# Kernel tuning notes

Measured on AMD Instinct MI355X. Metric: run time of the kernel, lower is better.

Reference implementation:

```python
import jax, jax.numpy as jnp
import numpy as np

N_TICKS = 550
N_PMTS = 12
SI = 47  # SiPM grid is 47x47 = 2209
BIN_SIGMA = 0.1
GAUSS_NORM = 1.0 / (BIN_SIGMA * 2.5066282746)


def _dense_init(k, fan_in, fan_out):
    lim = float(np.sqrt(6.0 / (fan_in + fan_out)))  # glorot_uniform (keras Dense default)
    W = jax.random.uniform(k, (fan_in, fan_out), jnp.float32, -lim, lim)
    b = jnp.zeros((fan_out,), jnp.float32)
    return W, b


def setup_inputs() -> dict:
    key = jax.random.key(0)
    ks = jax.random.split(key, 10)
    B, N = 4, 8192  # events x electrons-per-event (ragged list densified)
    xy = jax.random.normal(ks[0], (B, N, 2), jnp.float32)
    z = jax.random.uniform(ks[1], (B, N, 1), jnp.float32, minval=0.0, maxval=549.0)
    electrons = jnp.concatenate([xy, z], axis=-1)  # [B, N, 3] = (x, y, z_ticks)
    weight = jax.random.uniform(ks[2], (B, N), jnp.float32)  # lifetime survival weight
    Wp1, bp1 = _dense_init(ks[3], 2, 28)
    Wp2, bp2 = _dense_init(ks[4], 28, N_PMTS)
    Ws1, bs1 = _dense_init(ks[5], 2, 64)
    Ws2, bs2 = _dense_init(ks[6], 64, 128)
    Ws3, bs3 = _dense_init(ks[7], 128, 256)
    Ws4, bs4 = _dense_init(ks[8], 256, SI * SI)
    pmt_scale = jnp.ones((N_PMTS,), jnp.float32)
    si_scale = jnp.ones((SI * SI,), jnp.float32)
    return dict(electrons=electrons, weight=weight,
                Wp1=Wp1, bp1=bp1, Wp2=Wp2, bp2=bp2, pmt_scale=pmt_scale,
                Ws1=Ws1, bs1=bs1, Ws2=Ws2, bs2=bs2, Ws3=Ws3, bs3=bs3,
                Ws4=Ws4, bs4=bs4, si_scale=si_scale)


def reference(electrons, weight, Wp1, bp1, Wp2, bp2, pmt_scale,
              Ws1, bs1, Ws2, bs2, Ws3, bs3, Ws4, bs4, si_scale):
    B = electrons.shape[0]
    xy = electrons[..., 0:2]            # [B, N, 2]
    z = electrons[..., 2]               # [B, N] in tick units
    # tf.linspace(0.5, n_ticks-0.5, 550) == bin centers
    ticks = jnp.arange(N_TICKS, dtype=electrons.dtype) + 0.5  # [T]
    # per-electron Gaussian over time ticks, scaled by lifetime weight: [B, N, T]
    exp_values = (GAUSS_NORM
                  * jnp.exp(-(ticks - z[..., None]) ** 2 / BIN_SIGMA)
                  * weight[..., None])
    # PMT response MLP: 2 -> 28 -> 12, sigmoid activations
    h = jax.nn.sigmoid(xy @ Wp1 + bp1)
    pmt_resp = jax.nn.sigmoid(h @ Wp2 + bp2) * pmt_scale ** 2    # [B, N, 12]
    # sparse(hist)^T @ response, then transpose -> [B, 12, T]
    pmt_result = jnp.einsum('bnt,bnp->bpt', exp_values, pmt_resp)
    # SiPM response MLP: 2 -> 64 -> 128 -> 256 -> 2209, sigmoid activations
    s = jax.nn.sigmoid(xy @ Ws1 + bs1)
    s = jax.nn.sigmoid(s @ Ws2 + bs2)
    s = jax.nn.sigmoid(s @ Ws3 + bs3)
    sipm_resp = jax.nn.sigmoid(s @ Ws4 + bs4) * si_scale ** 2    # [B, N, 2209]
    sipm_result = jnp.einsum('bnt,bns->bst', exp_values, sipm_resp)  # [B, 2209, T]
    sipm_result = sipm_result.reshape(B, SI, SI, N_TICKS)
    return pmt_result, sipm_result
```

## Files before the change

### kernel.cpp

```cpp
#include <hip/hip_runtime.h>

typedef short short8 __attribute__((ext_vector_type(8)));
typedef short short4v __attribute__((ext_vector_type(4)));
typedef float f32x4 __attribute__((ext_vector_type(4)));

#define NT 550
#define NS 2209
#define NP 12
#define NBK 69
#define SC_NGRP 18
#define SC_GBK 4
#define SC_TW 32
#define NSG 139
#define G1_CPB 8
#define GNRM 3.9894228040143f

typedef unsigned short bfu;

__device__ __forceinline__ bfu f2bf(float f) {
    unsigned int u = __float_as_uint(f);
    unsigned int r = (u + 0x7fffu + ((u >> 16) & 1u)) >> 16;
    return (bfu)r;
}

__device__ __forceinline__ float sigm(float x) {
    return __builtin_amdgcn_rcpf(1.0f + __expf(-x));
}

__global__ void k_prep(const float* __restrict__ W2, const float* __restrict__ W3,
                       const float* __restrict__ W4,
                       bfu* __restrict__ w2h, bfu* __restrict__ w3h, bfu* __restrict__ w4h) {
    int id = blockIdx.x * 256 + threadIdx.x;
    if (id < 8192) {
        int c = id >> 6, k = id & 63;
        w2h[id] = f2bf(W2[k * 128 + c]);
    } else if (id < 8192 + 32768) {
        int j = id - 8192;
        int c = j >> 7, k = j & 127;
        w3h[j] = f2bf(W3[k * 256 + c]);
    } else {
        int j = id - 40960;
        int s = j >> 8, k = j & 255;
        w4h[j] = f2bf(s < NS ? W4[k * NS + s] : 0.0f);
    }
}

__global__ void k_count(const float* __restrict__ el, int* __restrict__ counts) {
    int id = blockIdx.x * 256 + threadIdx.x;
    float z = el[id * 3 + 2];
    int bk = (int)(z * 0.125f);
    bk = bk < 0 ? 0 : (bk > NBK - 1 ? NBK - 1 : bk);
    atomicAdd(&counts[(id >> 13) * NBK + bk], 1);
}

__global__ void k_scan(const int* __restrict__ counts, int* __restrict__ offs) {
    __shared__ int a[512];
    int tid = threadIdx.x;
    int v = (tid < 4 * NBK) ? counts[tid] : 0;
    a[tid] = v;
    __syncthreads();
    for (int s = 1; s < 512; s <<= 1) {
        int t = (tid >= s) ? a[tid - s] : 0;
        __syncthreads();
        a[tid] += t;
        __syncthreads();
    }
    if (tid < 4 * NBK) offs[tid] = a[tid] - v;
}

__global__ void k_scatter(const float* __restrict__ el, const float* __restrict__ wt,
                          const int* __restrict__ offs, int* __restrict__ cur,
                          int* __restrict__ inv, float4* __restrict__ elp) {
    int id = blockIdx.x * 256 + threadIdx.x;
    float x = el[id * 3], y = el[id * 3 + 1], z = el[id * 3 + 2];
    int bk = (int)(z * 0.125f);
    bk = bk < 0 ? 0 : (bk > NBK - 1 ? NBK - 1 : bk);
    int key = (id >> 13) * NBK + bk;
    int pos = offs[key] + atomicAdd(&cur[key], 1);
    inv[id] = pos;
    elp[pos] = make_float4(x, y, z, wt[id]);
}

__global__ __launch_bounds__(256, 1) void k_mlp(
    const float* __restrict__ el,
    const float* __restrict__ Ws1, const float* __restrict__ bs1,
    const float* __restrict__ bs2, const float* __restrict__ bs3,
    const bfu* __restrict__ w2h, const bfu* __restrict__ w3h,
    const int* __restrict__ inv, bfu* __restrict__ s3p) {

    __shared__ __align__(16) bfu bufA[32768];
    __shared__ __align__(16) bfu w3t[32768];
    __shared__ float xyb[256];
    __shared__ float s1w[128];
    __shared__ float b1s[64], b2s[128], b3s[256];

    bfu* h1t = bufA;
    bfu* w2t = bufA + 8192;
    bfu* h2t = bufA + 16384;

    const int tid = threadIdx.x;
    const int wv = tid >> 6, ln = tid & 63;
    const int e0 = blockIdx.x * 128;

    if (tid < 128) s1w[tid] = Ws1[tid];
    if (tid < 64) b1s[tid] = bs1[tid];
    if (tid < 128) b2s[tid] = bs2[tid];
    b3s[tid] = bs3[tid];

    if (tid < 128) {
        int e = e0 + tid;
        xyb[tid * 2] = el[e * 3]; xyb[tid * 2 + 1] = el[e * 3 + 1];
    }
    for (int i = 0; i < 4; ++i) {
        int cid = i * 256 + tid;
        int row = cid >> 3, c5 = cid & 7;
        short8 v = *(const short8*)(const void*)&w2h[row * 64 + c5 * 8];
        *(short8*)(void*)&w2t[row * 64 + ((c5 ^ (row & 7)) * 8)] = v;
    }
    for (int i = 0; i < 16; ++i) {
        int cid = i * 256 + tid;
        int row = cid >> 4, c5 = cid & 15;
        short8 v = *(const short8*)(const void*)&w3h[row * 128 + c5 * 8];
        *(short8*)(void*)&w3t[row * 128 + ((c5 ^ (row & 7)) * 8)] = v;
    }
    __syncthreads();

    {
        int n = tid & 127;
        int j0 = (tid >> 7) * 32;
        float xx = xyb[n * 2], yy = xyb[n * 2 + 1];
        for (int jj = 0; jj < 32; ++jj) {
            int j = j0 + jj;
            float h = sigm(xx * s1w[j] + yy * s1w[64 + j] + b1s[j]);
            h1t[n * 64 + (((j >> 3) ^ (n & 7)) * 8) + (j & 7)] = f2bf(h);
        }
    }
    __syncthreads();

    {
        const int mr = (wv >> 1) * 64;
        const int nc = (wv & 1) * 64;
        f32x4 acc[4][4];
        for (int m = 0; m < 4; ++m) for (int nf = 0; nf < 4; ++nf) acc[m][nf] = (f32x4){0.f, 0.f, 0.f, 0.f};
        for (int kk = 0; kk < 2; ++kk) {
            int kc = kk * 4 + (ln >> 4);
            short8 af[4], bf[4];
            for (int m = 0; m < 4; ++m) {
                int row = mr + 16 * m + (ln & 15);
                af[m] = *(const short8*)(const void*)&h1t[row * 64 + ((kc ^ (row & 7)) * 8)];
            }
            for (int nf = 0; nf < 4; ++nf) {
                int c = nc + 16 * nf + (ln & 15);
                bf[nf] = *(const short8*)(const void*)&w2t[c * 64 + ((kc ^ (c & 7)) * 8)];
            }
            for (int m = 0; m < 4; ++m)
                for (int nf = 0; nf < 4; ++nf)
                    acc[m][nf] = __builtin_amdgcn_mfma_f32_16x16x32_bf16(af[m], bf[nf], acc[m][nf], 0, 0, 0);
        }
        for (int m = 0; m < 4; ++m)
            for (int nf = 0; nf < 4; ++nf) {
                int c = nc + 16 * nf + (ln & 15);
                float bb = b2s[c];
                for (int r = 0; r < 4; ++r) {
                    int n = mr + 16 * m + (ln >> 4) * 4 + r;
                    float hh = sigm(acc[m][nf][r] + bb);
                    h2t[n * 128 + (((c >> 3) ^ (n & 7)) * 8) + (c & 7)] = f2bf(hh);
                }
            }
    }
    __syncthreads();

    f32x4 acc3[4][8];
    const int mr3 = (wv >> 1) * 64;
    const int nc3 = (wv & 1) * 128;
    for (int m = 0; m < 4; ++m) for (int nf = 0; nf < 8; ++nf) acc3[m][nf] = (f32x4){0.f, 0.f, 0.f, 0.f};
    for (int kk = 0; kk < 4; ++kk) {
        int kc = kk * 4 + (ln >> 4);
        short8 af[4];
        for (int m = 0; m < 4; ++m) {
            int row = mr3 + 16 * m + (ln & 15);
            af[m] = *(const short8*)(const void*)&h2t[row * 128 + ((kc ^ (row & 7)) * 8)];
        }
        for (int nf = 0; nf < 8; ++nf) {
            int c = nc3 + 16 * nf + (ln & 15);
            short8 bf = *(const short8*)(const void*)&w3t[c * 128 + ((kc ^ (c & 7)) * 8)];
            for (int m = 0; m < 4; ++m)
                acc3[m][nf] = __builtin_amdgcn_mfma_f32_16x16x32_bf16(af[m], bf, acc3[m][nf], 0, 0, 0);
        }
    }
    __syncthreads();
    for (int m = 0; m < 4; ++m)
        for (int nf = 0; nf < 8; ++nf) {
            int c = nc3 + 16 * nf + (ln & 15);
            float bb = b3s[c];
            for (int r = 0; r < 4; ++r) {
                int n = mr3 + 16 * m + (ln >> 4) * 4 + r;
                float ss = sigm(acc3[m][nf][r] + bb);
                bufA[n * 256 + (((c >> 3) ^ (n & 7)) * 8) + (c & 7)] = f2bf(ss);
            }
        }
    __syncthreads();
    for (int i = 0; i < 16; ++i) {
        int cid = i * 256 + tid;
        int row = cid >> 5, c5 = cid & 31;
        short8 v = *(const short8*)(const void*)&bufA[row * 256 + ((c5 ^ (row & 7)) * 8)];
        int dst = inv[e0 + row];
        *(short8*)(void*)&s3p[(size_t)dst * 256 + c5 * 8] = v;
    }
}

__global__ __launch_bounds__(512, 1) void k_g1(
    const float* __restrict__ bs4, const float* __restrict__ sis,
    const bfu* __restrict__ s3p, const bfu* __restrict__ w4h,
    bfu* __restrict__ resp) {

    __shared__ __align__(16) bfu s3t[128 * 256];
    __shared__ __align__(16) bfu rpt[128 * 128];

    const int tid = threadIdx.x;
    const int wv = tid >> 6, ln = tid & 63;
    const int st = blockIdx.x >> 5;
    const int cg = blockIdx.x & 31;
    const int s0 = st * 128;
    const int wn2 = (wv & 1) * 64;
    const int wsg = (wv >> 1) * 32;

    short8 bfr[2][8];
    float bssr[2], si2r[2];
#pragma unroll
    for (int nf = 0; nf < 2; ++nf) {
        int scol = s0 + wsg + 16 * nf + (ln & 15);
        const bfu* wp = &w4h[(size_t)scol * 256 + (ln >> 4) * 8];
#pragma unroll
        for (int kk = 0; kk < 8; ++kk)
            bfr[nf][kk] = *(const short8*)(const void*)&wp[kk * 32];
        bssr[nf] = (scol < NS) ? bs4[scol] : 0.0f;
        float sc = (scol < NS) ? sis[scol] : 0.0f;
        si2r[nf] = sc * sc;
    }

    const int rowS = tid >> 2;
    const int gq = tid & 3;
    const int r3 = rowS & 7;
    short8 rg0, rg1, rg2, rg3, rg4, rg5, rg6, rg7;

    {
        const bfu* p = s3p + ((size_t)(cg * G1_CPB) * 128 + rowS) * 256 + gq * 8;
        rg0 = *(const short8*)(const void*)&p[0];
        rg1 = *(const short8*)(const void*)&p[32];
        rg2 = *(const short8*)(const void*)&p[64];
        rg3 = *(const short8*)(const void*)&p[96];
        rg4 = *(const short8*)(const void*)&p[128];
        rg5 = *(const short8*)(const void*)&p[160];
        rg6 = *(const short8*)(const void*)&p[192];
        rg7 = *(const short8*)(const void*)&p[224];
    }

    for (int c = 0; c < G1_CPB; ++c) {
        {
            bfu* drow = s3t + rowS * 256;
            *(short8*)(void*)&drow[(((0 * 4 + gq) ^ r3) * 8)] = rg0;
            *(short8*)(void*)&drow[(((1 * 4 + gq) ^ r3) * 8)] = rg1;
            *(short8*)(void*)&drow[(((2 * 4 + gq) ^ r3) * 8)] = rg2;
            *(short8*)(void*)&drow[(((3 * 4 + gq) ^ r3) * 8)] = rg3;
            *(short8*)(void*)&drow[(((4 * 4 + gq) ^ r3) * 8)] = rg4;
            *(short8*)(void*)&drow[(((5 * 4 + gq) ^ r3) * 8)] = rg5;
            *(short8*)(void*)&drow[(((6 * 4 + gq) ^ r3) * 8)] = rg6;
            *(short8*)(void*)&drow[(((7 * 4 + gq) ^ r3) * 8)] = rg7;
        }
        __syncthreads();
        if (c + 1 < G1_CPB) {
            const bfu* p = s3p + ((size_t)(cg * G1_CPB + c + 1) * 128 + rowS) * 256 + gq * 8;
            rg0 = *(const short8*)(const void*)&p[0];
            rg1 = *(const short8*)(const void*)&p[32];
            rg2 = *(const short8*)(const void*)&p[64];
            rg3 = *(const short8*)(const void*)&p[96];
            rg4 = *(const short8*)(const void*)&p[128];
            rg5 = *(const short8*)(const void*)&p[160];
            rg6 = *(const short8*)(const void*)&p[192];
            rg7 = *(const short8*)(const void*)&p[224];
        }

        f32x4 acc[4][2];
#pragma unroll
        for (int m = 0; m < 4; ++m) {
            acc[m][0] = (f32x4){0.f,0.f,0.f,0.f};
            acc[m][1] = (f32x4){0.f,0.f,0.f,0.f};
        }
#pragma unroll
        for (int kk = 0; kk < 8; ++kk) {
            int kc = kk * 4 + (ln >> 4);
#pragma unroll
            for (int m = 0; m < 4; ++m) {
                int row = wn2 + 16 * m + (ln & 15);
                short8 am = *(const short8*)(const void*)&s3t[row * 256 + ((kc ^ (row & 7)) * 8)];
                acc[m][0] = __builtin_amdgcn_mfma_f32_16x16x32_bf16(am, bfr[0][kk], acc[m][0], 0, 0, 0);
                acc[m][1] = __builtin_amdgcn_mfma_f32_16x16x32_bf16(am, bfr[1][kk], acc[m][1], 0, 0, 0);
            }
        }
#pragma unroll
        for (int m = 0; m < 4; ++m) {
#pragma unroll
            for (int nf = 0; nf < 2; ++nf) {
                int scol = wsg + 16 * nf + (ln & 15);
                int n0 = wn2 + 16 * m + (ln >> 4) * 4;
                short4v pk;
#pragma unroll
                for (int r = 0; r < 4; ++r)
                    pk[r] = (short)f2bf(si2r[nf] * sigm(acc[m][nf][r] + bssr[nf]));
                *(short4v*)(void*)&rpt[scol * 128 + (((n0 >> 3) ^ (scol & 7)) * 8) + (n0 & 7)] = pk;
            }
        }
        __syncthreads();

        {
            size_t base = (size_t)(s0 + rowS) * 32768 + (size_t)(cg * G1_CPB + c) * 128;
            int r3w = rowS & 7;
#pragma unroll
            for (int i = 0; i < 4; ++i) {
                int g = i * 4 + gq;
                short8 v = *(const short8*)(const void*)&rpt[rowS * 128 + ((g ^ r3w) * 8)];
                *(short8*)(void*)&resp[base + g * 8] = v;
            }
        }
    }
}

__global__ void k_egen(const float4* __restrict__ elp, bfu* __restrict__ Eg) {
    int slot = blockIdx.x * 256 + threadIdx.x;
    float4 e4 = elp[slot];
    int bk = (int)(e4.z * 0.125f);
    bk = bk < 0 ? 0 : (bk > NBK - 1 ? NBK - 1 : bk);
    float wG = e4.w * GNRM;
#pragma unroll
    for (int j = 0; j < 16; ++j) {
        int tg = bk * 8 - 4 + j;
        float d = (float)tg + 0.5f - e4.z;
        float g = (tg >= 0 && tg < NT) ? wG * __expf(-10.0f * d * d) : 0.0f;
        Eg[j * 32768 + slot] = f2bf(g);
    }
}

__global__ void k_pmtresp(const float* __restrict__ el, const int* __restrict__ inv,
                          const float* __restrict__ Wp1, const float* __restrict__ bp1,
                          const float* __restrict__ Wp2, const float* __restrict__ bp2,
                          const float* __restrict__ psc, bfu* __restrict__ resp) {
    int id = blockIdx.x * 256 + threadIdx.x;
    float x = el[id * 3], y = el[id * 3 + 1];
    float hh[28];
#pragma unroll
    for (int j = 0; j < 28; ++j)
        hh[j] = sigm(x * Wp1[j] + y * Wp1[28 + j] + bp1[j]);
    int dst = inv[id];
#pragma unroll
    for (int p = 0; p < 12; ++p) {
        float a = bp2[p];
#pragma unroll
        for (int j = 0; j < 28; ++j) a += hh[j] * Wp2[j * 12 + p];
        float sc = psc[p];
        resp[(size_t)(NS + p) * 32768 + dst] = f2bf(sigm(a) * sc * sc);
    }
}

__global__ __launch_bounds__(256, 4) void k_scat(
    const bfu* __restrict__ Eg, const bfu* __restrict__ resp,
    const int* __restrict__ counts, const int* __restrict__ offs,
    float* __restrict__ outP, float* __restrict__ outS) {

    __shared__ float ring[4 * 16 * 17];

    const int tid = threadIdx.x;
    const int ln = tid & 63, wv = tid >> 6;
    const int wid = blockIdx.x * 4 + wv;
    const int sgrp = wid % NSG;
    const int grp  = (wid / NSG) % SC_NGRP;
    const int b    = wid / (NSG * SC_NGRP);

    const int bk0 = grp * SC_GBK;
    const int bk1 = (bk0 + SC_GBK < NBK) ? bk0 + SC_GBK : NBK;
    const int T_lo = bk0 * 8 - 2;
    const int scol = sgrp * 16 + (ln & 15);
    const bfu* rrow = resp + (size_t)scol * 32768;
    const bfu* erow = Eg + (size_t)(ln & 15) * 32768;
    float* ringw = ring + wv * 272;

    for (int i = ln; i < 272; i += 64) ringw[i] = 0.f;

    int F = 0;
    for (int bk = (bk0 > 0 ? bk0 - 1 : 0); bk < bk1; ++bk) {
        const int cnt = counts[b * NBK + bk];
        if (cnt == 0) continue;
        const int off = offs[b * NBK + bk];
        const int db8 = (bk - bk0) * 8;

        {
            int Fn = db8 - 2; Fn = Fn < 0 ? 0 : Fn;
            for (int tl = F + (ln >> 4); tl < Fn; tl += 4) {
                float v = ringw[(tl & 15) * 17 + (ln & 15)];
                ringw[(tl & 15) * 17 + (ln & 15)] = 0.f;
                int tg = T_lo + tl;
                if (tg >= 0 && tg < NT) {
                    if (scol < NS)
                        outS[((size_t)b * NS + scol) * NT + tg] = v;
                    else if (scol < NS + NP)
                        outP[((size_t)b * NP + (scol - NS)) * NT + tg] = v;
                }
            }
            F = (Fn > F) ? Fn : F;
        }

        const int off0 = off & ~31;
        const int nks = (off + cnt - off0 + 31) >> 5;
        const int hi = off + cnt;
        f32x4 acc = (f32x4){0.f, 0.f, 0.f, 0.f};
        for (int ks = 0; ks < nks; ++ks) {
            const int sb = off0 + ks * 32 + (ln >> 4) * 8;
            short8 af = *(const short8*)(const void*)&erow[sb];
            if ((ks == 0 && off0 < off) || (off0 + ks * 32 + 32 > hi)) {
#pragma unroll
                for (int j = 0; j < 8; ++j) {
                    int slot = sb + j;
                    if (slot < off || slot >= hi) af[j] = 0;
                }
            }
            short8 bb = *(const short8*)(const void*)&rrow[sb];
            acc = __builtin_amdgcn_mfma_f32_16x16x32_bf16(af, bb, acc, 0, 0, 0);
        }

#pragma unroll
        for (int r = 0; r < 4; ++r) {
            int tl = db8 - 2 + (ln >> 4) * 4 + r;
            if (tl >= 0 && tl < SC_TW)
                ringw[(tl & 15) * 17 + (ln & 15)] += acc[r];
        }
    }

    for (int tl = F + (ln >> 4); tl < SC_TW; tl += 4) {
        float v = ringw[(tl & 15) * 17 + (ln & 15)];
        int tg = T_lo + tl;
        if (tg >= 0 && tg < NT) {
            if (scol < NS)
                outS[((size_t)b * NS + scol) * NT + tg] = v;
            else if (scol < NS + NP)
                outP[((size_t)b * NP + (scol - NS)) * NT + tg] = v;
        }
    }
}

extern "C" void kernel_launch(void* const* d_in, const int* in_sizes, int n_in,
                              void* d_out, int out_size, void* d_ws, size_t ws_size,
                              hipStream_t stream) {
    const float* el  = (const float*)d_in[0];
    const float* wt  = (const float*)d_in[1];
    const float* Wp1 = (const float*)d_in[2];
    const float* bp1 = (const float*)d_in[3];
    const float* Wp2 = (const float*)d_in[4];
    const float* bp2 = (const float*)d_in[5];
    const float* psc = (const float*)d_in[6];
    const float* Ws1 = (const float*)d_in[7];
    const float* bs1 = (const float*)d_in[8];
    const float* Ws2 = (const float*)d_in[9];
    const float* bs2 = (const float*)d_in[10];
    const float* Ws3 = (const float*)d_in[11];
    const float* bs3 = (const float*)d_in[12];
    const float* Ws4 = (const float*)d_in[13];
    const float* bs4 = (const float*)d_in[14];
    const float* sis = (const float*)d_in[15];
    float* out = (float*)d_out;

    char* ws = (char*)d_ws;
    bfu* w2h     = (bfu*)(ws);
    bfu* w3h     = (bfu*)(ws + 16384);
    bfu* w4h     = (bfu*)(ws + 81920);
    bfu* Eg      = (bfu*)(ws + 81920);
    bfu* s3p     = (bfu*)(ws + 1261568);
    int* counts  = (int*)(ws + 18038784);
    int* offs    = (int*)(ws + 18042880);
    int* cursors = (int*)(ws + 18046976);
    int* inv     = (int*)(ws + 18051072);
    float4* elp  = (float4*)(ws + 18182144);
    bfu* resp    = (bfu*)(ws + 18706432);

    hipMemsetAsync(counts, 0, 4096, stream);
    hipMemsetAsync(cursors, 0, 4096, stream);

    k_prep<<<2464, 256, 0, stream>>>(Ws2, Ws3, Ws4, w2h, w3h, w4h);
    k_count<<<128, 256, 0, stream>>>(el, counts);
    k_scan<<<1, 512, 0, stream>>>(counts, offs);
    k_scatter<<<128, 256, 0, stream>>>(el, wt, offs, cursors, inv, elp);
    k_mlp<<<256, 256, 0, stream>>>(el, Ws1, bs1, bs2, bs3, w2h, w3h, inv, s3p);
    k_g1<<<18 * 32, 512, 0, stream>>>(bs4, sis, s3p, w4h, resp);
    k_egen<<<128, 256, 0, stream>>>(elp, Eg);
    k_pmtresp<<<128, 256, 0, stream>>>(el, inv, Wp1, bp1, Wp2, bp2, psc, resp);
    k_scat<<<(4 * SC_NGRP * NSG) / 4, 256, 0, stream>>>(Eg, resp, counts, offs,
                                                        out, out + 4 * NP * NT);
}
```

Before: 221.1 us.

## Fuse SiPM response GEMM with time-scatter GEMM, accumulating via ring and atomics

The SiPM response tile produced in shared memory by the layer-4 GEMM is consumed directly by the time-histogram MFMA in the same kernel. This removes the write and re-read of the large bf16 response matrix in global memory. Partial sums are kept in a shared-memory ring buffer and flushed to the output with float atomicAdd, so the output now has to be zeroed first. PMT handling moves to a small separate scatter kernel. The costs are atomic traffic, the extra memset of the full output, and more shared memory per block.

```diff
diff --git a/kernel.cpp b/kernel.cpp
--- a/kernel.cpp
+++ b/kernel.cpp
@@ -8,10 +8,7 @@
 #define NS 2209
 #define NP 12
 #define NBK 69
-#define SC_NGRP 18
-#define SC_GBK 4
-#define SC_TW 32
-#define NSG 139
+#define NKEY 276
 #define G1_CPB 8
 #define GNRM 3.9894228040143f
 
@@ -56,7 +53,7 @@
 __global__ void k_scan(const int* __restrict__ counts, int* __restrict__ offs) {
     __shared__ int a[512];
     int tid = threadIdx.x;
-    int v = (tid < 4 * NBK) ? counts[tid] : 0;
+    int v = (tid < NKEY) ? counts[tid] : 0;
     a[tid] = v;
     __syncthreads();
     for (int s = 1; s < 512; s <<= 1) {
@@ -65,7 +62,7 @@
         a[tid] += t;
         __syncthreads();
     }
-    if (tid < 4 * NBK) offs[tid] = a[tid] - v;
+    if (tid < NKEY) offs[tid] = a[tid] - v;
 }
 
 __global__ void k_scatter(const float* __restrict__ el, const float* __restrict__ wt,
@@ -81,6 +78,21 @@
     elp[pos] = make_float4(x, y, z, wt[id]);
 }
 
+__global__ void k_egen(const float4* __restrict__ elp, bfu* __restrict__ Eg) {
+    int slot = blockIdx.x * 256 + threadIdx.x;
+    float4 e4 = elp[slot];
+    int bk = (int)(e4.z * 0.125f);
+    bk = bk < 0 ? 0 : (bk > NBK - 1 ? NBK - 1 : bk);
+    float wG = e4.w * GNRM;
+#pragma unroll
+    for (int j = 0; j < 16; ++j) {
+        int tg = bk * 8 - 4 + j;
+        float d = (float)tg + 0.5f - e4.z;
+        float g = (tg >= 0 && tg < NT) ? wG * __expf(-10.0f * d * d) : 0.0f;
+        Eg[j * 32768 + slot] = f2bf(g);
+    }
+}
+
 __global__ __launch_bounds__(256, 1) void k_mlp(
     const float* __restrict__ el,
     const float* __restrict__ Ws1, const float* __restrict__ bs1,
@@ -209,13 +221,37 @@
     }
 }
 
-__global__ __launch_bounds__(512, 1) void k_g1(
+__global__ void k_pmtresp(const float* __restrict__ el, const int* __restrict__ inv,
+                          const float* __restrict__ Wp1, const float* __restrict__ bp1,
+                          const float* __restrict__ Wp2, const float* __restrict__ bp2,
+                          const float* __restrict__ psc, bfu* __restrict__ respP) {
+    int id = blockIdx.x * 256 + threadIdx.x;
+    float x = el[id * 3], y = el[id * 3 + 1];
+    float hh[28];
+#pragma unroll
+    for (int j = 0; j < 28; ++j)
+        hh[j] = sigm(x * Wp1[j] + y * Wp1[28 + j] + bp1[j]);
+    int dst = inv[id];
+#pragma unroll
+    for (int p = 0; p < 12; ++p) {
+        float a = bp2[p];
+#pragma unroll
+        for (int j = 0; j < 28; ++j) a += hh[j] * Wp2[j * 12 + p];
+        float sc = psc[p];
+        respP[(size_t)p * 32768 + dst] = f2bf(sigm(a) * sc * sc);
+    }
+}
+
+__global__ __launch_bounds__(512, 1) void k_fuse(
     const float* __restrict__ bs4, const float* __restrict__ sis,
     const bfu* __restrict__ s3p, const bfu* __restrict__ w4h,
-    bfu* __restrict__ resp) {
+    const bfu* __restrict__ Eg, const int* __restrict__ offs,
+    float* __restrict__ outS) {
 
     __shared__ __align__(16) bfu s3t[128 * 256];
     __shared__ __align__(16) bfu rpt[128 * 128];
+    __shared__ float ring[64 * 132];
+    __shared__ int ofl[NKEY + 1];
 
     const int tid = threadIdx.x;
     const int wv = tid >> 6, ln = tid & 63;
@@ -224,6 +260,13 @@
     const int s0 = st * 128;
     const int wn2 = (wv & 1) * 64;
     const int wsg = (wv >> 1) * 32;
+    const int sg2 = wv * 16 + (ln & 15);
+    const int cb0 = cg * 1024;
+    const bfu* erow = Eg + (size_t)(ln & 15) * 32768;
+
+    for (int i = tid; i < NKEY; i += 512) ofl[i] = offs[i];
+    if (tid == 0) ofl[NKEY] = 32768;
+    for (int i = tid; i < 64 * 132; i += 512) ring[i] = 0.f;
 
     short8 bfr[2][8];
     float bssr[2], si2r[2];
@@ -243,9 +286,8 @@
     const int gq = tid & 3;
     const int r3 = rowS & 7;
     short8 rg0, rg1, rg2, rg3, rg4, rg5, rg6, rg7;
-
     {
-        const bfu* p = s3p + ((size_t)(cg * G1_CPB) * 128 + rowS) * 256 + gq * 8;
+        const bfu* p = s3p + ((size_t)cb0 * 256) + (size_t)rowS * 256 + gq * 8;
         rg0 = *(const short8*)(const void*)&p[0];
         rg1 = *(const short8*)(const void*)&p[32];
         rg2 = *(const short8*)(const void*)&p[64];
@@ -255,8 +297,13 @@
         rg6 = *(const short8*)(const void*)&p[192];
         rg7 = *(const short8*)(const void*)&p[224];
     }
+    __syncthreads();
+
+    int key = 0, F = 0, maxk = 0;
+    bool first = true;
 
     for (int c = 0; c < G1_CPB; ++c) {
+        const int cb = cb0 + c * 128;
         {
             bfu* drow = s3t + rowS * 256;
             *(short8*)(void*)&drow[(((0 * 4 + gq) ^ r3) * 8)] = rg0;
@@ -269,8 +316,31 @@
             *(short8*)(void*)&drow[(((7 * 4 + gq) ^ r3) * 8)] = rg7;
         }
         __syncthreads();
+
+        while (ofl[key + 1] <= cb) ++key;
+        if (first) { F = key * 8 - 4; first = false; }
+        {
+            int limit = key * 8 - 4;
+            if (limit > F) {
+                for (int i = tid; i < (limit - F) * 128; i += 512) {
+                    int dvt = i >> 7, s = i & 127;
+                    int vt = F + dvt;
+                    float v = ring[(vt & 63) * 132 + s];
+                    ring[(vt & 63) * 132 + s] = 0.f;
+                    if (vt >= 0 && v != 0.f) {
+                        int b = vt / 552;
+                        int tg = vt - b * 552;
+                        int sg = s0 + s;
+                        if (b < 4 && tg < NT && sg < NS)
+                            atomicAdd(&outS[((size_t)b * NS + sg) * NT + tg], v);
+                    }
+                }
+                F = limit;
+            }
+        }
+
         if (c + 1 < G1_CPB) {
-            const bfu* p = s3p + ((size_t)(cg * G1_CPB + c + 1) * 128 + rowS) * 256 + gq * 8;
+            const bfu* p = s3p + ((size_t)(cb0 + (c + 1) * 128) * 256) + (size_t)rowS * 256 + gq * 8;
             rg0 = *(const short8*)(const void*)&p[0];
             rg1 = *(const short8*)(const void*)&p[32];
             rg2 = *(const short8*)(const void*)&p[64];
@@ -314,74 +384,74 @@
         __syncthreads();
 
         {
-            size_t base = (size_t)(s0 + rowS) * 32768 + (size_t)(cg * G1_CPB + c) * 128;
-            int r3w = rowS & 7;
-#pragma unroll
-            for (int i = 0; i < 4; ++i) {
-                int g = i * 4 + gq;
-                short8 v = *(const short8*)(const void*)&rpt[rowS * 128 + ((g ^ r3w) * 8)];
-                *(short8*)(void*)&resp[base + g * 8] = v;
-            }
-        }
-    }
-}
-
-__global__ void k_egen(const float4* __restrict__ elp, bfu* __restrict__ Eg) {
-    int slot = blockIdx.x * 256 + threadIdx.x;
-    float4 e4 = elp[slot];
-    int bk = (int)(e4.z * 0.125f);
-    bk = bk < 0 ? 0 : (bk > NBK - 1 ? NBK - 1 : bk);
-    float wG = e4.w * GNRM;
-#pragma unroll
-    for (int j = 0; j < 16; ++j) {
-        int tg = bk * 8 - 4 + j;
-        float d = (float)tg + 0.5f - e4.z;
-        float g = (tg >= 0 && tg < NT) ? wG * __expf(-10.0f * d * d) : 0.0f;
-        Eg[j * 32768 + slot] = f2bf(g);
-    }
-}
-
-__global__ void k_pmtresp(const float* __restrict__ el, const int* __restrict__ inv,
-                          const float* __restrict__ Wp1, const float* __restrict__ bp1,
-                          const float* __restrict__ Wp2, const float* __restrict__ bp2,
-                          const float* __restrict__ psc, bfu* __restrict__ resp) {
-    int id = blockIdx.x * 256 + threadIdx.x;
-    float x = el[id * 3], y = el[id * 3 + 1];
-    float hh[28];
-#pragma unroll
-    for (int j = 0; j < 28; ++j)
-        hh[j] = sigm(x * Wp1[j] + y * Wp1[28 + j] + bp1[j]);
-    int dst = inv[id];
-#pragma unroll
-    for (int p = 0; p < 12; ++p) {
-        float a = bp2[p];
-#pragma unroll
-        for (int j = 0; j < 28; ++j) a += hh[j] * Wp2[j * 12 + p];
-        float sc = psc[p];
-        resp[(size_t)(NS + p) * 32768 + dst] = f2bf(sigm(a) * sc * sc);
-    }
-}
-
-__global__ __launch_bounds__(256, 4) void k_scat(
-    const bfu* __restrict__ Eg, const bfu* __restrict__ resp,
+            int k2 = key;
+            while (k2 < NKEY && ofl[k2] < cb + 128) {
+                int lo = ofl[k2] > cb ? ofl[k2] : cb;
+                int hi = ofl[k2 + 1] < cb + 128 ? ofl[k2 + 1] : cb + 128;
+                if (lo < hi) {
+                    f32x4 a2 = (f32x4){0.f,0.f,0.f,0.f};
+                    int ksl = (lo - cb) >> 5, ksh = (hi - 1 - cb) >> 5;
+                    for (int ks = ksl; ks <= ksh; ++ks) {
+                        int sb = cb + ks * 32 + (ln >> 4) * 8;
+                        short8 af = *(const short8*)(const void*)&erow[sb];
+                        if (cb + ks * 32 < lo || cb + ks * 32 + 32 > hi) {
+#pragma unroll
+                            for (int j = 0; j < 8; ++j) {
+                                int slot = sb + j;
+                                if (slot < lo || slot >= hi) af[j] = 0;
+                            }
+                        }
+                        int kc = ks * 4 + (ln >> 4);
+                        short8 bb = *(const short8*)(const void*)&rpt[sg2 * 128 + ((kc ^ (sg2 & 7)) * 8)];
+                        a2 = __builtin_amdgcn_mfma_f32_16x16x32_bf16(af, bb, a2, 0, 0, 0);
+                    }
+                    int vtb = k2 * 8 - 4 + (ln >> 4) * 4;
+#pragma unroll
+                    for (int r = 0; r < 4; ++r)
+                        ring[((vtb + r) & 63) * 132 + sg2] += a2[r];
+                }
+                ++k2;
+            }
+            maxk = k2;
+        }
+    }
+
+    __syncthreads();
+    {
+        int limit = maxk * 8 + 4;
+        for (int i = tid; i < (limit - F) * 128; i += 512) {
+            int dvt = i >> 7, s = i & 127;
+            int vt = F + dvt;
+            float v = ring[(vt & 63) * 132 + s];
+            if (vt >= 0 && v != 0.f) {
+                int b = vt / 552;
+                int tg = vt - b * 552;
+                int sg = s0 + s;
+                if (b < 4 && tg < NT && sg < NS)
+                    atomicAdd(&outS[((size_t)b * NS + sg) * NT + tg], v);
+            }
+        }
+    }
+}
+
+__global__ __launch_bounds__(256, 4) void k_pscat(
+    const bfu* __restrict__ Eg, const bfu* __restrict__ respP,
     const int* __restrict__ counts, const int* __restrict__ offs,
-    float* __restrict__ outP, float* __restrict__ outS) {
+    float* __restrict__ outP) {
 
     __shared__ float ring[4 * 16 * 17];
 
     const int tid = threadIdx.x;
     const int ln = tid & 63, wv = tid >> 6;
     const int wid = blockIdx.x * 4 + wv;
-    const int sgrp = wid % NSG;
-    const int grp  = (wid / NSG) % SC_NGRP;
-    const int b    = wid / (NSG * SC_NGRP);
-
-    const int bk0 = grp * SC_GBK;
-    const int bk1 = (bk0 + SC_GBK < NBK) ? bk0 + SC_GBK : NBK;
+    const int grp = wid % 18;
+    const int b   = wid / 18;
+    const int bk0 = grp * 4;
+    const int bk1 = (bk0 + 4 < NBK) ? bk0 + 4 : NBK;
     const int T_lo = bk0 * 8 - 2;
-    const int scol = sgrp * 16 + (ln & 15);
-    const bfu* rrow = resp + (size_t)scol * 32768;
-    const bfu* erow = Eg + (size_t)(ln & 15) * 32768;
+    const int p = ln & 15;
+    const bfu* rrow = respP + (size_t)p * 32768;
+    const bfu* erow = Eg + (size_t)p * 32768;
     float* ringw = ring + wv * 272;
 
     for (int i = ln; i < 272; i += 64) ringw[i] = 0.f;
@@ -396,15 +466,11 @@
         {
             int Fn = db8 - 2; Fn = Fn < 0 ? 0 : Fn;
             for (int tl = F + (ln >> 4); tl < Fn; tl += 4) {
-                float v = ringw[(tl & 15) * 17 + (ln & 15)];
-                ringw[(tl & 15) * 17 + (ln & 15)] = 0.f;
+                float v = ringw[(tl & 15) * 17 + p];
+                ringw[(tl & 15) * 17 + p] = 0.f;
                 int tg = T_lo + tl;
-                if (tg >= 0 && tg < NT) {
-                    if (scol < NS)
-                        outS[((size_t)b * NS + scol) * NT + tg] = v;
-                    else if (scol < NS + NP)
-                        outP[((size_t)b * NP + (scol - NS)) * NT + tg] = v;
-                }
+                if (tg >= 0 && tg < NT && p < NP)
+                    outP[((size_t)b * NP + p) * NT + tg] = v;
             }
             F = (Fn > F) ? Fn : F;
         }
@@ -426,24 +492,19 @@
             short8 bb = *(const short8*)(const void*)&rrow[sb];
             acc = __builtin_amdgcn_mfma_f32_16x16x32_bf16(af, bb, acc, 0, 0, 0);
         }
-
 #pragma unroll
         for (int r = 0; r < 4; ++r) {
             int tl = db8 - 2 + (ln >> 4) * 4 + r;
-            if (tl >= 0 && tl < SC_TW)
-                ringw[(tl & 15) * 17 + (ln & 15)] += acc[r];
-        }
-    }
-
-    for (int tl = F + (ln >> 4); tl < SC_TW; tl += 4) {
-        float v = ringw[(tl & 15) * 17 + (ln & 15)];
+            if (tl >= 0 && tl < 32)
+                ringw[(tl & 15) * 17 + p] += acc[r];
+        }
+    }
+
+    for (int tl = F + (ln >> 4); tl < 32; tl += 4) {
+        float v = ringw[(tl & 15) * 17 + p];
         int tg = T_lo + tl;
-        if (tg >= 0 && tg < NT) {
-            if (scol < NS)
-                outS[((size_t)b * NS + scol) * NT + tg] = v;
-            else if (scol < NS + NP)
-                outP[((size_t)b * NP + (scol - NS)) * NT + tg] = v;
-        }
+        if (tg >= 0 && tg < NT && p < NP)
+            outP[((size_t)b * NP + p) * NT + tg] = v;
     }
 }
 
@@ -472,15 +533,16 @@
     bfu* w2h     = (bfu*)(ws);
     bfu* w3h     = (bfu*)(ws + 16384);
     bfu* w4h     = (bfu*)(ws + 81920);
-    bfu* Eg      = (bfu*)(ws + 81920);
     bfu* s3p     = (bfu*)(ws + 1261568);
     int* counts  = (int*)(ws + 18038784);
     int* offs    = (int*)(ws + 18042880);
     int* cursors = (int*)(ws + 18046976);
     int* inv     = (int*)(ws + 18051072);
     float4* elp  = (float4*)(ws + 18182144);
-    bfu* resp    = (bfu*)(ws + 18706432);
-
+    bfu* respP   = (bfu*)(ws + 18706432);
+    bfu* Eg      = (bfu*)(ws + 19755008);
+
+    hipMemsetAsync(out, 0, (size_t)out_size * 4, stream);
     hipMemsetAsync(counts, 0, 4096, stream);
     hipMemsetAsync(cursors, 0, 4096, stream);
 
@@ -488,10 +550,9 @@
     k_count<<<128, 256, 0, stream>>>(el, counts);
     k_scan<<<1, 512, 0, stream>>>(counts, offs);
     k_scatter<<<128, 256, 0, stream>>>(el, wt, offs, cursors, inv, elp);
+    k_egen<<<128, 256, 0, stream>>>(elp, Eg);
     k_mlp<<<256, 256, 0, stream>>>(el, Ws1, bs1, bs2, bs3, w2h, w3h, inv, s3p);
-    k_g1<<<18 * 32, 512, 0, stream>>>(bs4, sis, s3p, w4h, resp);
-    k_egen<<<128, 256, 0, stream>>>(elp, Eg);
-    k_pmtresp<<<128, 256, 0, stream>>>(el, inv, Wp1, bp1, Wp2, bp2, psc, resp);
-    k_scat<<<(4 * SC_NGRP * NSG) / 4, 256, 0, stream>>>(Eg, resp, counts, offs,
-                                                        out, out + 4 * NP * NT);
-}
+    k_pmtresp<<<128, 256, 0, stream>>>(el, inv, Wp1, bp1, Wp2, bp2, psc, respP);
+    k_fuse<<<18 * 32, 512, 0, stream>>>(bs4, sis, s3p, w4h, Eg, offs, out + 4 * NP * NT);
+    k_pscat<<<18, 256, 0, stream>>>(Eg, respP, counts, offs, out);
+}
```

Measured after the change: 436.9 us. +97.6%, slower.

## Double-buffer g1 staging, store responses directly, and split scatter MFMA accumulators

Applied to the files above, without the earlier changes.

The SiPM output-layer GEMM kernel now processes 64-row chunks with a double-buffered LDS tile instead of 128-row chunks. The next chunk's global load and LDS write overlap the current MFMA work, and one barrier per chunk is removed. The LDS transpose buffer for responses is dropped, so sigmoid results go straight to global memory as 8-byte stores, which may coalesce less well than the old 16-byte row stores. Less LDS lets two blocks run per CU. Separately, the scatter kernel's K loop is unrolled by two with independent accumulators to break the MFMA dependency chain.

```diff
diff --git a/kernel.cpp b/kernel.cpp
--- a/kernel.cpp
+++ b/kernel.cpp
@@ -12,7 +12,6 @@
 #define SC_GBK 4
 #define SC_TW 32
 #define NSG 139
-#define G1_CPB 8
 #define GNRM 3.9894228040143f
 
 typedef unsigned short bfu;
@@ -209,21 +208,21 @@
     }
 }
 
-__global__ __launch_bounds__(512, 1) void k_g1(
+__global__ __launch_bounds__(512, 2) void k_g1(
     const float* __restrict__ bs4, const float* __restrict__ sis,
     const bfu* __restrict__ s3p, const bfu* __restrict__ w4h,
     bfu* __restrict__ resp) {
 
-    __shared__ __align__(16) bfu s3t[128 * 256];
-    __shared__ __align__(16) bfu rpt[128 * 128];
+    __shared__ __align__(16) bfu s3t[2][64 * 256];
 
     const int tid = threadIdx.x;
     const int wv = tid >> 6, ln = tid & 63;
     const int st = blockIdx.x >> 5;
     const int cg = blockIdx.x & 31;
     const int s0 = st * 128;
-    const int wn2 = (wv & 1) * 64;
+    const int wn2 = (wv & 1) * 32;
     const int wsg = (wv >> 1) * 32;
+    const int slot00 = cg * 1024;
 
     short8 bfr[2][8];
     float bssr[2], si2r[2];
@@ -239,90 +238,71 @@
         si2r[nf] = sc * sc;
     }
 
-    const int rowS = tid >> 2;
-    const int gq = tid & 3;
+    const int rowS = tid >> 3;
+    const int gq = tid & 7;
     const int r3 = rowS & 7;
-    short8 rg0, rg1, rg2, rg3, rg4, rg5, rg6, rg7;
-
-    {
-        const bfu* p = s3p + ((size_t)(cg * G1_CPB) * 128 + rowS) * 256 + gq * 8;
+    short8 rg0, rg1, rg2, rg3;
+
+    auto ISSUE = [&](int c) {
+        const bfu* p = s3p + ((size_t)(slot00 + c * 64 + rowS)) * 256 + gq * 8;
         rg0 = *(const short8*)(const void*)&p[0];
-        rg1 = *(const short8*)(const void*)&p[32];
-        rg2 = *(const short8*)(const void*)&p[64];
-        rg3 = *(const short8*)(const void*)&p[96];
-        rg4 = *(const short8*)(const void*)&p[128];
-        rg5 = *(const short8*)(const void*)&p[160];
-        rg6 = *(const short8*)(const void*)&p[192];
-        rg7 = *(const short8*)(const void*)&p[224];
-    }
-
-    for (int c = 0; c < G1_CPB; ++c) {
-        {
-            bfu* drow = s3t + rowS * 256;
-            *(short8*)(void*)&drow[(((0 * 4 + gq) ^ r3) * 8)] = rg0;
-            *(short8*)(void*)&drow[(((1 * 4 + gq) ^ r3) * 8)] = rg1;
-            *(short8*)(void*)&drow[(((2 * 4 + gq) ^ r3) * 8)] = rg2;
-            *(short8*)(void*)&drow[(((3 * 4 + gq) ^ r3) * 8)] = rg3;
-            *(short8*)(void*)&drow[(((4 * 4 + gq) ^ r3) * 8)] = rg4;
-            *(short8*)(void*)&drow[(((5 * 4 + gq) ^ r3) * 8)] = rg5;
-            *(short8*)(void*)&drow[(((6 * 4 + gq) ^ r3) * 8)] = rg6;
-            *(short8*)(void*)&drow[(((7 * 4 + gq) ^ r3) * 8)] = rg7;
-        }
-        __syncthreads();
-        if (c + 1 < G1_CPB) {
-            const bfu* p = s3p + ((size_t)(cg * G1_CPB + c + 1) * 128 + rowS) * 256 + gq * 8;
-            rg0 = *(const short8*)(const void*)&p[0];
-            rg1 = *(const short8*)(const void*)&p[32];
-            rg2 = *(const short8*)(const void*)&p[64];
-            rg3 = *(const short8*)(const void*)&p[96];
-            rg4 = *(const short8*)(const void*)&p[128];
-            rg5 = *(const short8*)(const void*)&p[160];
-            rg6 = *(const short8*)(const void*)&p[192];
-            rg7 = *(const short8*)(const void*)&p[224];
-        }
-
-        f32x4 acc[4][2];
-#pragma unroll
-        for (int m = 0; m < 4; ++m) {
-            acc[m][0] = (f32x4){0.f,0.f,0.f,0.f};
-            acc[m][1] = (f32x4){0.f,0.f,0.f,0.f};
-        }
+        rg1 = *(const short8*)(const void*)&p[64];
+        rg2 = *(const short8*)(const void*)&p[128];
+        rg3 = *(const short8*)(const void*)&p[192];
+    };
+    auto WSTAGE = [&](int buf) {
+        bfu* drow = s3t[buf] + rowS * 256;
+        *(short8*)(void*)&drow[(((0 * 8 + gq) ^ r3) * 8)] = rg0;
+        *(short8*)(void*)&drow[(((1 * 8 + gq) ^ r3) * 8)] = rg1;
+        *(short8*)(void*)&drow[(((2 * 8 + gq) ^ r3) * 8)] = rg2;
+        *(short8*)(void*)&drow[(((3 * 8 + gq) ^ r3) * 8)] = rg3;
+    };
+
+    ISSUE(0); WSTAGE(0);
+    __syncthreads();
+
+    for (int c = 0; c < 16; ++c) {
+        if (c + 1 < 16) ISSUE(c + 1);
+
+        const bfu* sb = s3t[c & 1];
+        f32x4 acc00 = (f32x4){0.f,0.f,0.f,0.f};
+        f32x4 acc01 = (f32x4){0.f,0.f,0.f,0.f};
+        f32x4 acc10 = (f32x4){0.f,0.f,0.f,0.f};
+        f32x4 acc11 = (f32x4){0.f,0.f,0.f,0.f};
+        const int ar0 = wn2 + (ln & 15), ar1 = wn2 + 16 + (ln & 15);
 #pragma unroll
         for (int kk = 0; kk < 8; ++kk) {
             int kc = kk * 4 + (ln >> 4);
-#pragma unroll
-            for (int m = 0; m < 4; ++m) {
-                int row = wn2 + 16 * m + (ln & 15);
-                short8 am = *(const short8*)(const void*)&s3t[row * 256 + ((kc ^ (row & 7)) * 8)];
-                acc[m][0] = __builtin_amdgcn_mfma_f32_16x16x32_bf16(am, bfr[0][kk], acc[m][0], 0, 0, 0);
-                acc[m][1] = __builtin_amdgcn_mfma_f32_16x16x32_bf16(am, bfr[1][kk], acc[m][1], 0, 0, 0);
-            }
-        }
-#pragma unroll
-        for (int m = 0; m < 4; ++m) {
-#pragma unroll
-            for (int nf = 0; nf < 2; ++nf) {
-                int scol = wsg + 16 * nf + (ln & 15);
-                int n0 = wn2 + 16 * m + (ln >> 4) * 4;
-                short4v pk;
-#pragma unroll
-                for (int r = 0; r < 4; ++r)
-                    pk[r] = (short)f2bf(si2r[nf] * sigm(acc[m][nf][r] + bssr[nf]));
-                *(short4v*)(void*)&rpt[scol * 128 + (((n0 >> 3) ^ (scol & 7)) * 8) + (n0 & 7)] = pk;
-            }
+            short8 a0 = *(const short8*)(const void*)&sb[ar0 * 256 + ((kc ^ (ar0 & 7)) * 8)];
+            short8 a1 = *(const short8*)(const void*)&sb[ar1 * 256 + ((kc ^ (ar1 & 7)) * 8)];
+            acc00 = __builtin_amdgcn_mfma_f32_16x16x32_bf16(a0, bfr[0][kk], acc00, 0, 0, 0);
+            acc01 = __builtin_amdgcn_mfma_f32_16x16x32_bf16(a0, bfr[1][kk], acc01, 0, 0, 0);
+            acc10 = __builtin_amdgcn_mfma_f32_16x16x32_bf16(a1, bfr[0][kk], acc10, 0, 0, 0);
+            acc11 = __builtin_amdgcn_mfma_f32_16x16x32_bf16(a1, bfr[1][kk], acc11, 0, 0, 0);
+        }
+        if (c + 1 < 16) WSTAGE((c + 1) & 1);
+
+        {
+            int sc0 = s0 + wsg + (ln & 15);
+            int sc1 = sc0 + 16;
+            int base = slot00 + c * 64;
+            int n0a = base + wn2 + (ln >> 4) * 4;
+            int n0b = n0a + 16;
+            short4v pk;
+#pragma unroll
+            for (int r = 0; r < 4; ++r) pk[r] = (short)f2bf(si2r[0] * sigm(acc00[r] + bssr[0]));
+            *(short4v*)(void*)&resp[(size_t)sc0 * 32768 + n0a] = pk;
+#pragma unroll
+            for (int r = 0; r < 4; ++r) pk[r] = (short)f2bf(si2r[1] * sigm(acc01[r] + bssr[1]));
+            *(short4v*)(void*)&resp[(size_t)sc1 * 32768 + n0a] = pk;
+#pragma unroll
+            for (int r = 0; r < 4; ++r) pk[r] = (short)f2bf(si2r[0] * sigm(acc10[r] + bssr[0]));
+            *(short4v*)(void*)&resp[(size_t)sc0 * 32768 + n0b] = pk;
+#pragma unroll
+            for (int r = 0; r < 4; ++r) pk[r] = (short)f2bf(si2r[1] * sigm(acc11[r] + bssr[1]));
+            *(short4v*)(void*)&resp[(size_t)sc1 * 32768 + n0b] = pk;
         }
         __syncthreads();
-
-        {
-            size_t base = (size_t)(s0 + rowS) * 32768 + (size_t)(cg * G1_CPB + c) * 128;
-            int r3w = rowS & 7;
-#pragma unroll
-            for (int i = 0; i < 4; ++i) {
-                int g = i * 4 + gq;
-                short8 v = *(const short8*)(const void*)&rpt[rowS * 128 + ((g ^ r3w) * 8)];
-                *(short8*)(void*)&resp[base + g * 8] = v;
-            }
-        }
     }
 }
 
@@ -413,25 +393,47 @@
         const int nks = (off + cnt - off0 + 31) >> 5;
         const int hi = off + cnt;
         f32x4 acc = (f32x4){0.f, 0.f, 0.f, 0.f};
-        for (int ks = 0; ks < nks; ++ks) {
-            const int sb = off0 + ks * 32 + (ln >> 4) * 8;
-            short8 af = *(const short8*)(const void*)&erow[sb];
+        f32x4 acc1 = (f32x4){0.f, 0.f, 0.f, 0.f};
+        int ks = 0;
+        for (; ks + 1 < nks; ks += 2) {
+            const int sb0 = off0 + ks * 32 + (ln >> 4) * 8;
+            const int sb1 = sb0 + 32;
+            short8 af0 = *(const short8*)(const void*)&erow[sb0];
+            short8 af1 = *(const short8*)(const void*)&erow[sb1];
+            short8 bb0 = *(const short8*)(const void*)&rrow[sb0];
+            short8 bb1 = *(const short8*)(const void*)&rrow[sb1];
+            if (ks == 0 && off0 < off) {
+#pragma unroll
+                for (int j = 0; j < 8; ++j) { int slot = sb0 + j; if (slot < off) af0[j] = 0; }
+            }
+            if (off0 + ks * 32 + 64 > hi) {
+#pragma unroll
+                for (int j = 0; j < 8; ++j) { int slot = sb0 + j; if (slot >= hi) af0[j] = 0; }
+#pragma unroll
+                for (int j = 0; j < 8; ++j) { int slot = sb1 + j; if (slot >= hi) af1[j] = 0; }
+            }
+            acc  = __builtin_amdgcn_mfma_f32_16x16x32_bf16(af0, bb0, acc, 0, 0, 0);
+            acc1 = __builtin_amdgcn_mfma_f32_16x16x32_bf16(af1, bb1, acc1, 0, 0, 0);
+        }
+        if (ks < nks) {
+            const int sb0 = off0 + ks * 32 + (ln >> 4) * 8;
+            short8 af0 = *(const short8*)(const void*)&erow[sb0];
+            short8 bb0 = *(const short8*)(const void*)&rrow[sb0];
             if ((ks == 0 && off0 < off) || (off0 + ks * 32 + 32 > hi)) {
 #pragma unroll
                 for (int j = 0; j < 8; ++j) {
-                    int slot = sb + j;
-                    if (slot < off || slot >= hi) af[j] = 0;
+                    int slot = sb0 + j;
+                    if (slot < off || slot >= hi) af0[j] = 0;
                 }
             }
-            short8 bb = *(const short8*)(const void*)&rrow[sb];
-            acc = __builtin_amdgcn_mfma_f32_16x16x32_bf16(af, bb, acc, 0, 0, 0);
+            acc = __builtin_amdgcn_mfma_f32_16x16x32_bf16(af0, bb0, acc, 0, 0, 0);
         }
 
 #pragma unroll
         for (int r = 0; r < 4; ++r) {
             int tl = db8 - 2 + (ln >> 4) * 4 + r;
             if (tl >= 0 && tl < SC_TW)
-                ringw[(tl & 15) * 17 + (ln & 15)] += acc[r];
+                ringw[(tl & 15) * 17 + (ln & 15)] += acc[r] + acc1[r];
         }
     }
 
```

Result: no change. 220.4 us (-0.3%).
